# Performance work log

Measured on AMD Instinct MI355X. Metric: run time of the kernel, lower is better.

The kernel has to match this reference:

```python
import jax, jax.numpy as jnp
import numpy as np

L, B, D = 512, 32, 256  # seq_len, batch (hardcoded 32 in source), in_size == hidden_size
H = D


def setup_inputs() -> dict:
    key = jax.random.key(0)
    ks = jax.random.split(key, 9)
    s_in = 1.0 / np.sqrt(D)
    s_h = 1.0 / np.sqrt(H)
    return {
        "v": jax.random.normal(ks[0], (L, B, D), jnp.float32),
        "h0": jax.random.normal(ks[1], (B, H), jnp.float32),       # torch.randn h
        "Vvec": jax.random.normal(ks[2], (B, H), jnp.float32),     # torch.randn V (squeezed [B,H,1])
        "Wp": jax.random.normal(ks[3], (H, D), jnp.float32) * s_in,   # nn.Linear(D,H,bias=False).weight
        "Wp_": jax.random.normal(ks[4], (H, D), jnp.float32) * s_in,
        "W_ih": jax.random.normal(ks[5], (3 * H, D), jnp.float32) * s_h,  # GRUCell weight_ih
        "W_hh": jax.random.normal(ks[6], (3 * H, H), jnp.float32) * s_h,
        "b_ih": jax.random.normal(ks[7], (3 * H,), jnp.float32) * s_h,
        "b_hh": jax.random.normal(ks[8], (3 * H,), jnp.float32) * s_h,
    }


def _gru_cell(c, h, W_ih, W_hh, b_ih, b_hh):
    # torch.nn.GRUCell math
    gi = c @ W_ih.T + b_ih   # [B, 3H]
    gh = h @ W_hh.T + b_hh   # [B, 3H]
    i_r, i_z, i_n = jnp.split(gi, 3, axis=1)
    h_r, h_z, h_n = jnp.split(gh, 3, axis=1)
    r = jax.nn.sigmoid(i_r + h_r)
    z = jax.nn.sigmoid(i_z + h_z)
    n = jnp.tanh(i_n + r * h_n)
    return (1.0 - z) * n + z * h


def reference(v, h0, Vvec, Wp, Wp_, W_ih, W_hh, b_ih, b_hh):
    # Hoist the two linear projections out of the scan (they don't depend on h).
    xq = jnp.einsum('lbd,hd->lbh', v, Wp)    # Wp(v[i]) for all i
    xv = jnp.einsum('lbd,hd->lbh', v, Wp_)   # Wp_(v), reused every step

    def step(h, xq_i):
        x = jnp.tanh(xq_i[None, :, :] + xv)          # [L, B, H]
        s = jnp.einsum('lbh,bh->bl', x, Vvec)        # attention scores over L
        a = jax.nn.softmax(s, axis=1)                # [B, L]
        c = jnp.einsum('bl,lbd->bd', a, v)           # context [B, D]
        h_new = _gru_cell(c, h, W_ih, W_hh, b_ih, b_hh)
        return h_new, h_new

    _, hs = jax.lax.scan(step, h0, xq)  # hs: [L, B, H]
    # dropout is identity in eval mode
    return hs
```

## Files before the change

kernel.cpp:

```cpp
#include <hip/hip_runtime.h>
#include <stdint.h>


#define C2    2.8853900817779268f
#define LOG2E 1.4426950408889634f

typedef __fp16 f16x2 __attribute__((ext_vector_type(2)));
typedef __fp16 f16x4_t __attribute__((ext_vector_type(4)));
typedef __fp16 f16x8 __attribute__((ext_vector_type(8)));
typedef float f32x4 __attribute__((ext_vector_type(4)));

static __device__ __forceinline__ float rcp_f(float x)  { return __builtin_amdgcn_rcpf(x); }
static __device__ __forceinline__ float exp2_f(float x) { return __builtin_amdgcn_exp2f(x); }

__global__ __launch_bounds__(256) void gemm_nt(
    const float* __restrict__ A, const float* __restrict__ W,
    const float* __restrict__ bias, float* __restrict__ out,
    int N, int expmode)
{
  __shared__ __align__(16) float As[32][68];
  __shared__ __align__(16) float Ws[32][68];
  const int t = threadIdx.x;
  const int tx = t & 15, ty = t >> 4;
  const int n0 = blockIdx.x * 64, m0 = blockIdx.y * 64;
  float acc[4][4] = {};

  for (int k0 = 0; k0 < 256; k0 += 32) {
#pragma unroll
    for (int s = 0; s < 2; ++s) {
      int f = t + s * 256;
      int row = f >> 3, kq = f & 7;
      float4 a = *(const float4*)&A[(size_t)(m0 + row) * 256 + k0 + kq * 4];
      float4 w = *(const float4*)&W[(size_t)(n0 + row) * 256 + k0 + kq * 4];
      As[kq * 4 + 0][row] = a.x; As[kq * 4 + 1][row] = a.y;
      As[kq * 4 + 2][row] = a.z; As[kq * 4 + 3][row] = a.w;
      Ws[kq * 4 + 0][row] = w.x; Ws[kq * 4 + 1][row] = w.y;
      Ws[kq * 4 + 2][row] = w.z; Ws[kq * 4 + 3][row] = w.w;
    }
    __syncthreads();
#pragma unroll
    for (int kk = 0; kk < 32; ++kk) {
      float4 a4 = *(const float4*)&As[kk][ty * 4];
      float4 b4 = *(const float4*)&Ws[kk][tx * 4];
      float av[4] = {a4.x, a4.y, a4.z, a4.w};
      float bv[4] = {b4.x, b4.y, b4.z, b4.w};
#pragma unroll
      for (int r = 0; r < 4; ++r)
#pragma unroll
        for (int c = 0; c < 4; ++c)
          acc[r][c] = fmaf(av[r], bv[c], acc[r][c]);
    }
    __syncthreads();
  }

#pragma unroll
  for (int r = 0; r < 4; ++r) {
    float4 o;
    if (expmode) {
      o.x = exp2_f(C2 * acc[r][0]); o.y = exp2_f(C2 * acc[r][1]);
      o.z = exp2_f(C2 * acc[r][2]); o.w = exp2_f(C2 * acc[r][3]);
    } else {
      float4 bb = *(const float4*)&bias[n0 + tx * 4];
      o.x = acc[r][0] + bb.x; o.y = acc[r][1] + bb.y;
      o.z = acc[r][2] + bb.z; o.w = acc[r][3] + bb.w;
    }
    *(float4*)&out[(size_t)(m0 + ty * 4 + r) * N + n0 + tx * 4] = o;
  }
}

__global__ __launch_bounds__(256) void gemm_gi(
    const float* __restrict__ A, const float* __restrict__ W,
    const float* __restrict__ bih, const float* __restrict__ bhh,
    __fp16* __restrict__ G)
{
  __shared__ __align__(16) float As[32][68];
  __shared__ __align__(16) float Ws[32][68];
  const int t = threadIdx.x;
  const int tx = t & 15, ty = t >> 4;
  const int n0 = blockIdx.x * 64, m0 = blockIdx.y * 64;
  float acc[4][4] = {};

  for (int k0 = 0; k0 < 256; k0 += 32) {
#pragma unroll
    for (int s = 0; s < 2; ++s) {
      int f = t + s * 256;
      int row = f >> 3, kq = f & 7;
      float4 a = *(const float4*)&A[(size_t)(m0 + row) * 256 + k0 + kq * 4];
      float4 w = *(const float4*)&W[(size_t)(n0 + row) * 256 + k0 + kq * 4];
      As[kq * 4 + 0][row] = a.x; As[kq * 4 + 1][row] = a.y;
      As[kq * 4 + 2][row] = a.z; As[kq * 4 + 3][row] = a.w;
      Ws[kq * 4 + 0][row] = w.x; Ws[kq * 4 + 1][row] = w.y;
      Ws[kq * 4 + 2][row] = w.z; Ws[kq * 4 + 3][row] = w.w;
    }
    __syncthreads();
#pragma unroll
    for (int kk = 0; kk < 32; ++kk) {
      float4 a4 = *(const float4*)&As[kk][ty * 4];
      float4 b4 = *(const float4*)&Ws[kk][tx * 4];
      float av[4] = {a4.x, a4.y, a4.z, a4.w};
      float bv[4] = {b4.x, b4.y, b4.z, b4.w};
#pragma unroll
      for (int r = 0; r < 4; ++r)
#pragma unroll
        for (int c = 0; c < 4; ++c)
          acc[r][c] = fmaf(av[r], bv[c], acc[r][c]);
    }
    __syncthreads();
  }

  float bias[4];
#pragma unroll
  for (int c = 0; c < 4; ++c) {
    int n = n0 + tx * 4 + c;
    bias[c] = bih[n] + (n < 512 ? bhh[n] : 0.f);
  }
#pragma unroll
  for (int r = 0; r < 4; ++r) {
    int m = m0 + ty * 4 + r;
    f16x4_t o;
#pragma unroll
    for (int c = 0; c < 4; ++c) o[c] = (__fp16)(acc[r][c] + bias[c]);
    *(f16x4_t*)&G[(size_t)m * 768 + n0 + tx * 4] = o;
  }
}

__global__ __launch_bounds__(256) void score_k(
    const float* __restrict__ Eq, const float* __restrict__ Ev,
    const float* __restrict__ Vvec, float* __restrict__ S)
{
  __shared__ __align__(16) float Eqs[64][68];
  __shared__ __align__(16) float Evs[32][68];
  __shared__ __align__(16) float Vs[256];
  const int t = threadIdx.x;
  const int tx = t & 15, ty = t >> 4;
  const int l0 = blockIdx.x * 32;
  const int i0 = blockIdx.y * 64;
  const int b  = blockIdx.z;

  Vs[t] = -2.0f * Vvec[b * 256 + t];
  float acc[4][2] = {};

  for (int st = 0; st < 4; ++st) {
    const int h0 = st * 64;
#pragma unroll
    for (int s = 0; s < 4; ++s) {
      int f = t + s * 256;
      int row = f >> 4, cq = f & 15;
      *(float4*)&Eqs[row][cq * 4] =
          *(const float4*)&Eq[((size_t)(i0 + row) * 32 + b) * 256 + h0 + cq * 4];
    }
#pragma unroll
    for (int s = 0; s < 2; ++s) {
      int f = t + s * 256;
      int row = f >> 4, cq = f & 15;
      *(float4*)&Evs[row][cq * 4] =
          *(const float4*)&Ev[((size_t)(l0 + row) * 32 + b) * 256 + h0 + cq * 4];
    }
    __syncthreads();
#pragma unroll 4
    for (int k4 = 0; k4 < 16; ++k4) {
      float4 vh = *(const float4*)&Vs[h0 + k4 * 4];
      float4 e0 = *(const float4*)&Evs[tx][k4 * 4];
      float4 e1 = *(const float4*)&Evs[tx + 16][k4 * 4];
#pragma unroll
      for (int r = 0; r < 4; ++r) {
        float4 eq = *(const float4*)&Eqs[ty * 4 + r][k4 * 4];
        acc[r][0] += vh.x * rcp_f(fmaf(eq.x, e0.x, 1.0f));
        acc[r][0] += vh.y * rcp_f(fmaf(eq.y, e0.y, 1.0f));
        acc[r][0] += vh.z * rcp_f(fmaf(eq.z, e0.z, 1.0f));
        acc[r][0] += vh.w * rcp_f(fmaf(eq.w, e0.w, 1.0f));
        acc[r][1] += vh.x * rcp_f(fmaf(eq.x, e1.x, 1.0f));
        acc[r][1] += vh.y * rcp_f(fmaf(eq.y, e1.y, 1.0f));
        acc[r][1] += vh.z * rcp_f(fmaf(eq.z, e1.z, 1.0f));
        acc[r][1] += vh.w * rcp_f(fmaf(eq.w, e1.w, 1.0f));
      }
    }
    __syncthreads();
  }

#pragma unroll
  for (int r = 0; r < 4; ++r) {
    float* ps = &S[((size_t)b * 512 + i0 + ty * 4 + r) * 512 + l0];
    ps[tx]      = acc[r][0];
    ps[tx + 16] = acc[r][1];
  }
}

__global__ __launch_bounds__(64) void softmax_k(float* __restrict__ S)
{
  const int t = threadIdx.x;
  float* row = &S[(size_t)blockIdx.x * 512];
  float x[8];
  float m = -1e30f;
#pragma unroll
  for (int u = 0; u < 8; ++u) { x[u] = row[t + u * 64]; m = fmaxf(m, x[u]); }
#pragma unroll
  for (int o = 32; o; o >>= 1) m = fmaxf(m, __shfl_xor(m, o, 64));
  float sum = 0.f;
#pragma unroll
  for (int u = 0; u < 8; ++u) { x[u] = exp2_f(LOG2E * (x[u] - m)); sum += x[u]; }
#pragma unroll
  for (int o = 32; o; o >>= 1) sum += __shfl_xor(sum, o, 64);
  float inv = rcp_f(sum);
#pragma unroll
  for (int u = 0; u < 8; ++u) row[t + u * 64] = x[u] * inv;
}

__global__ __launch_bounds__(256) void ctx_k(
    const float* __restrict__ Aw, const float* __restrict__ v,
    float* __restrict__ C)
{
  __shared__ __align__(16) float As[32][68];
  __shared__ __align__(16) float Vs[32][68];
  const int t = threadIdx.x, tx = t & 15, ty = t >> 4;
  const int d0 = blockIdx.x * 64, i0 = blockIdx.y * 64, b = blockIdx.z;
  float acc[4][4] = {};

  for (int l0 = 0; l0 < 512; l0 += 32) {
#pragma unroll
    for (int s = 0; s < 2; ++s) {
      int f = t + s * 256;
      int row = f >> 3, lq = f & 7;
      float4 a = *(const float4*)&Aw[((size_t)b * 512 + i0 + row) * 512 + l0 + lq * 4];
      As[lq * 4 + 0][row] = a.x; As[lq * 4 + 1][row] = a.y;
      As[lq * 4 + 2][row] = a.z; As[lq * 4 + 3][row] = a.w;
    }
#pragma unroll
    for (int s = 0; s < 2; ++s) {
      int f = t + s * 256;
      int row = f >> 4, dq = f & 15;
      *(float4*)&Vs[row][dq * 4] =
          *(const float4*)&v[((size_t)(l0 + row) * 32 + b) * 256 + d0 + dq * 4];
    }
    __syncthreads();
#pragma unroll
    for (int kk = 0; kk < 32; ++kk) {
      float4 a4 = *(const float4*)&As[kk][ty * 4];
      float4 b4 = *(const float4*)&Vs[kk][tx * 4];
      float av[4] = {a4.x, a4.y, a4.z, a4.w};
      float bv[4] = {b4.x, b4.y, b4.z, b4.w};
#pragma unroll
      for (int r = 0; r < 4; ++r)
#pragma unroll
        for (int c = 0; c < 4; ++c)
          acc[r][c] = fmaf(av[r], bv[c], acc[r][c]);
    }
    __syncthreads();
  }

#pragma unroll
  for (int r = 0; r < 4; ++r) {
    float4 o = {acc[r][0], acc[r][1], acc[r][2], acc[r][3]};
    *(float4*)&C[((size_t)(i0 + ty * 4 + r) * 32 + b) * 256 + d0 + tx * 4] = o;
  }
}

__global__ __launch_bounds__(512, 1) void gru_k(
    const __fp16* __restrict__ Gi2, const float* __restrict__ Whh,
    const float* __restrict__ bhh, const float* __restrict__ h0,
    float* __restrict__ out)
{
  __shared__ __align__(16) __fp16 hA[2][256];
  const int t = threadIdx.x, wave = t >> 6, lane = t & 63;
  const int quad = lane >> 4, col = lane & 15;
  const int b = blockIdx.x;
  const int jw = wave * 32;

  f16x8 Bf[2][3][8];
#pragma unroll
  for (int p = 0; p < 2; ++p)
#pragma unroll
    for (int g = 0; g < 3; ++g) {
      const float* wrow = &Whh[(size_t)(g * 256 + jw + p * 16 + col) * 256];
#pragma unroll
      for (int kk = 0; kk < 8; ++kk) {
        const float4* wp = (const float4*)&wrow[kk * 32 + quad * 8];
        float4 w0 = wp[0], w1 = wp[1];
        f16x8 f;
        f[0] = (__fp16)w0.x; f[1] = (__fp16)w0.y;
        f[2] = (__fp16)w0.z; f[3] = (__fp16)w0.w;
        f[4] = (__fp16)w1.x; f[5] = (__fp16)w1.y;
        f[6] = (__fp16)w1.z; f[7] = (__fp16)w1.w;
        Bf[p][g][kk] = f;
      }
    }

  float hold[2];
  float bn[2];
#pragma unroll
  for (int p = 0; p < 2; ++p) {
    int j = jw + p * 16 + col;
    bn[p] = bhh[512 + j];
    float h = h0[(size_t)b * 256 + j];
    hold[p] = h;
    if (quad == 0) hA[0][j] = (__fp16)h;
  }
  __syncthreads();

  __fp16 gcur[2][3];
#pragma unroll
  for (int p = 0; p < 2; ++p)
#pragma unroll
    for (int g = 0; g < 3; ++g)
      gcur[p][g] = Gi2[(size_t)b * 768 + g * 256 + jw + p * 16 + col];

  for (int i = 0; i < 512; ++i) {
    __fp16 gnext[2][3];
    {
      int ip = (i + 1 < 512) ? (i + 1) : 511;
#pragma unroll
      for (int p = 0; p < 2; ++p)
#pragma unroll
        for (int g = 0; g < 3; ++g)
          gnext[p][g] =
              Gi2[(size_t)(ip * 32 + b) * 768 + g * 256 + jw + p * 16 + col];
    }

    f32x4 acc[2][3];
#pragma unroll
    for (int p = 0; p < 2; ++p)
#pragma unroll
      for (int g = 0; g < 3; ++g)
        acc[p][g] = (f32x4){0.f, 0.f, 0.f, 0.f};

    const __fp16* hbuf = hA[i & 1];
#pragma unroll
    for (int kk = 0; kk < 8; ++kk) {
      f16x8 a = *(const f16x8*)&hbuf[kk * 32 + quad * 8];
#pragma unroll
      for (int p = 0; p < 2; ++p)
#pragma unroll
        for (int g = 0; g < 3; ++g)
          acc[p][g] = __builtin_amdgcn_mfma_f32_16x16x32_f16(
              a, Bf[p][g][kk], acc[p][g], 0, 0, 0);
    }

    __fp16* hnext = hA[(i + 1) & 1];
#pragma unroll
    for (int p = 0; p < 2; ++p) {
      int j = jw + p * 16 + col;
      float rr = rcp_f(1.f + exp2_f(-LOG2E * ((float)gcur[p][0] + acc[p][0][0])));
      float zz = rcp_f(1.f + exp2_f(-LOG2E * ((float)gcur[p][1] + acc[p][1][0])));
      float na = fmaf(rr, acc[p][2][0] + bn[p], (float)gcur[p][2]);
      float nn = fmaf(-2.f, rcp_f(1.f + exp2_f(C2 * na)), 1.f);
      float h = fmaf(zz, hold[p] - nn, nn);
      hold[p] = h;
      if (quad == 0) {
        out[((size_t)i * 32 + b) * 256 + j] = h;
        hnext[j] = (__fp16)h;
      }
    }
#pragma unroll
    for (int p = 0; p < 2; ++p)
#pragma unroll
      for (int g = 0; g < 3; ++g) gcur[p][g] = gnext[p][g];
    __syncthreads();
  }
}

extern "C" void kernel_launch(void* const* d_in, const int* in_sizes, int n_in,
                              void* d_out, int out_size, void* d_ws, size_t ws_size,
                              hipStream_t stream)
{
  const float* v   = (const float*)d_in[0];
  const float* h0  = (const float*)d_in[1];
  const float* Vv  = (const float*)d_in[2];
  const float* Wp  = (const float*)d_in[3];
  const float* Wp_ = (const float*)d_in[4];
  const float* Wih = (const float*)d_in[5];
  const float* Whh = (const float*)d_in[6];
  const float* bih = (const float*)d_in[7];
  const float* bhh = (const float*)d_in[8];
  float* out = (float*)d_out;
  float* ws  = (float*)d_ws;

  float* Eq = ws;
  float* Ev = ws + 4194304;
  float* S  = ws + 8388608;
  float* C  = ws;
  __fp16* Gi2 = (__fp16*)(ws + 4194304);

  gemm_nt<<<dim3(4, 256), 256, 0, stream>>>(v, Wp,  nullptr, Eq, 256, 1);
  gemm_nt<<<dim3(4, 256), 256, 0, stream>>>(v, Wp_, nullptr, Ev, 256, 1);
  score_k<<<dim3(16, 8, 32), 256, 0, stream>>>(Eq, Ev, Vv, S);
  softmax_k<<<16384, 64, 0, stream>>>(S);
  ctx_k<<<dim3(4, 8, 32), 256, 0, stream>>>(S, v, C);
  gemm_gi<<<dim3(12, 256), 256, 0, stream>>>(C, Wih, bih, bhh, Gi2);
  gru_k<<<32, 512, 0, stream>>>(Gi2, Whh, bhh, h0, out);
}
```

Baseline: 1.058 ms.

## Move projection, context and input-gate GEMMs to fp16 MFMA and fuse projections

Replaces the scalar FP32 tiled GEMMs for the two attention projections, the context product and the GRU input gates with fp16 MFMA 16x16x32 kernels. Operands are converted to half precision while staging into shared memory. The two projection GEMMs are fused into one kernel so v is loaded once, and softmax now packs four rows per 256-thread block with float4 loads. The cost is lower operand precision in these GEMMs, plus transposed fp16 shared-memory stores for v in the context kernel.

```diff
diff --git a/kernel.cpp b/kernel.cpp
--- a/kernel.cpp
+++ b/kernel.cpp
@@ -5,123 +5,166 @@
 #define C2    2.8853900817779268f
 #define LOG2E 1.4426950408889634f
 
-typedef __fp16 f16x2 __attribute__((ext_vector_type(2)));
 typedef __fp16 f16x4_t __attribute__((ext_vector_type(4)));
 typedef __fp16 f16x8 __attribute__((ext_vector_type(8)));
 typedef float f32x4 __attribute__((ext_vector_type(4)));
 
 static __device__ __forceinline__ float rcp_f(float x)  { return __builtin_amdgcn_rcpf(x); }
 static __device__ __forceinline__ float exp2_f(float x) { return __builtin_amdgcn_exp2f(x); }
-
-__global__ __launch_bounds__(256) void gemm_nt(
-    const float* __restrict__ A, const float* __restrict__ W,
-    const float* __restrict__ bias, float* __restrict__ out,
-    int N, int expmode)
-{
-  __shared__ __align__(16) float As[32][68];
-  __shared__ __align__(16) float Ws[32][68];
-  const int t = threadIdx.x;
-  const int tx = t & 15, ty = t >> 4;
+static __device__ __forceinline__ f16x8 cvt8(float4 a, float4 b) {
+  f16x8 f;
+  f[0] = (__fp16)a.x; f[1] = (__fp16)a.y; f[2] = (__fp16)a.z; f[3] = (__fp16)a.w;
+  f[4] = (__fp16)b.x; f[5] = (__fp16)b.y; f[6] = (__fp16)b.z; f[7] = (__fp16)b.w;
+  return f;
+}
+
+
+__global__ __launch_bounds__(256) void proj_k(
+    const float* __restrict__ v, const float* __restrict__ Wp,
+    const float* __restrict__ Wp_, float* __restrict__ Eq,
+    float* __restrict__ Ev)
+{
+  __shared__ __align__(16) __fp16 As[64][40];
+  __shared__ __align__(16) __fp16 Wqs[64][40];
+  __shared__ __align__(16) __fp16 Wvs[64][40];
+  const int t = threadIdx.x, wave = t >> 6, lane = t & 63;
+  const int quad = lane >> 4, col = lane & 15;
   const int n0 = blockIdx.x * 64, m0 = blockIdx.y * 64;
-  float acc[4][4] = {};
-
-  for (int k0 = 0; k0 < 256; k0 += 32) {
-#pragma unroll
-    for (int s = 0; s < 2; ++s) {
-      int f = t + s * 256;
-      int row = f >> 3, kq = f & 7;
-      float4 a = *(const float4*)&A[(size_t)(m0 + row) * 256 + k0 + kq * 4];
-      float4 w = *(const float4*)&W[(size_t)(n0 + row) * 256 + k0 + kq * 4];
-      As[kq * 4 + 0][row] = a.x; As[kq * 4 + 1][row] = a.y;
-      As[kq * 4 + 2][row] = a.z; As[kq * 4 + 3][row] = a.w;
-      Ws[kq * 4 + 0][row] = w.x; Ws[kq * 4 + 1][row] = w.y;
-      Ws[kq * 4 + 2][row] = w.z; Ws[kq * 4 + 3][row] = w.w;
-    }
-    __syncthreads();
-#pragma unroll
-    for (int kk = 0; kk < 32; ++kk) {
-      float4 a4 = *(const float4*)&As[kk][ty * 4];
-      float4 b4 = *(const float4*)&Ws[kk][tx * 4];
-      float av[4] = {a4.x, a4.y, a4.z, a4.w};
-      float bv[4] = {b4.x, b4.y, b4.z, b4.w};
-#pragma unroll
-      for (int r = 0; r < 4; ++r)
-#pragma unroll
-        for (int c = 0; c < 4; ++c)
-          acc[r][c] = fmaf(av[r], bv[c], acc[r][c]);
-    }
-    __syncthreads();
-  }
-
-#pragma unroll
-  for (int r = 0; r < 4; ++r) {
-    float4 o;
-    if (expmode) {
-      o.x = exp2_f(C2 * acc[r][0]); o.y = exp2_f(C2 * acc[r][1]);
-      o.z = exp2_f(C2 * acc[r][2]); o.w = exp2_f(C2 * acc[r][3]);
-    } else {
-      float4 bb = *(const float4*)&bias[n0 + tx * 4];
-      o.x = acc[r][0] + bb.x; o.y = acc[r][1] + bb.y;
-      o.z = acc[r][2] + bb.z; o.w = acc[r][3] + bb.w;
-    }
-    *(float4*)&out[(size_t)(m0 + ty * 4 + r) * N + n0 + tx * 4] = o;
-  }
-}
-
-__global__ __launch_bounds__(256) void gemm_gi(
+  const int srow = t >> 2, skq = t & 3;
+
+  f32x4 accq[4], accv[4];
+#pragma unroll
+  for (int nt = 0; nt < 4; ++nt) {
+    accq[nt] = (f32x4){0.f, 0.f, 0.f, 0.f};
+    accv[nt] = (f32x4){0.f, 0.f, 0.f, 0.f};
+  }
+
+  for (int kc = 0; kc < 8; ++kc) {
+    const int k0 = kc * 32;
+    {
+      const float4* ap = (const float4*)&v[(size_t)(m0 + srow) * 256 + k0 + skq * 8];
+      *(f16x8*)&As[srow][skq * 8] = cvt8(ap[0], ap[1]);
+      const float4* qp = (const float4*)&Wp[(size_t)(n0 + srow) * 256 + k0 + skq * 8];
+      *(f16x8*)&Wqs[srow][skq * 8] = cvt8(qp[0], qp[1]);
+      const float4* vp = (const float4*)&Wp_[(size_t)(n0 + srow) * 256 + k0 + skq * 8];
+      *(f16x8*)&Wvs[srow][skq * 8] = cvt8(vp[0], vp[1]);
+    }
+    __syncthreads();
+    f16x8 a = *(const f16x8*)&As[wave * 16 + col][quad * 8];
+#pragma unroll
+    for (int nt = 0; nt < 4; ++nt) {
+      f16x8 bq = *(const f16x8*)&Wqs[nt * 16 + col][quad * 8];
+      f16x8 bv = *(const f16x8*)&Wvs[nt * 16 + col][quad * 8];
+      accq[nt] = __builtin_amdgcn_mfma_f32_16x16x32_f16(a, bq, accq[nt], 0, 0, 0);
+      accv[nt] = __builtin_amdgcn_mfma_f32_16x16x32_f16(a, bv, accv[nt], 0, 0, 0);
+    }
+    __syncthreads();
+  }
+
+#pragma unroll
+  for (int nt = 0; nt < 4; ++nt)
+#pragma unroll
+    for (int r = 0; r < 4; ++r) {
+      size_t m = m0 + wave * 16 + quad * 4 + r;
+      size_t n = n0 + nt * 16 + col;
+      Eq[m * 256 + n] = exp2_f(C2 * accq[nt][r]);
+      Ev[m * 256 + n] = exp2_f(C2 * accv[nt][r]);
+    }
+}
+
+__global__ __launch_bounds__(256) void gi_k(
     const float* __restrict__ A, const float* __restrict__ W,
     const float* __restrict__ bih, const float* __restrict__ bhh,
     __fp16* __restrict__ G)
 {
-  __shared__ __align__(16) float As[32][68];
-  __shared__ __align__(16) float Ws[32][68];
-  const int t = threadIdx.x;
-  const int tx = t & 15, ty = t >> 4;
+  __shared__ __align__(16) __fp16 As[64][40];
+  __shared__ __align__(16) __fp16 Ws[64][40];
+  const int t = threadIdx.x, wave = t >> 6, lane = t & 63;
+  const int quad = lane >> 4, col = lane & 15;
   const int n0 = blockIdx.x * 64, m0 = blockIdx.y * 64;
-  float acc[4][4] = {};
-
-  for (int k0 = 0; k0 < 256; k0 += 32) {
-#pragma unroll
-    for (int s = 0; s < 2; ++s) {
-      int f = t + s * 256;
-      int row = f >> 3, kq = f & 7;
-      float4 a = *(const float4*)&A[(size_t)(m0 + row) * 256 + k0 + kq * 4];
-      float4 w = *(const float4*)&W[(size_t)(n0 + row) * 256 + k0 + kq * 4];
-      As[kq * 4 + 0][row] = a.x; As[kq * 4 + 1][row] = a.y;
-      As[kq * 4 + 2][row] = a.z; As[kq * 4 + 3][row] = a.w;
-      Ws[kq * 4 + 0][row] = w.x; Ws[kq * 4 + 1][row] = w.y;
-      Ws[kq * 4 + 2][row] = w.z; Ws[kq * 4 + 3][row] = w.w;
-    }
-    __syncthreads();
-#pragma unroll
-    for (int kk = 0; kk < 32; ++kk) {
-      float4 a4 = *(const float4*)&As[kk][ty * 4];
-      float4 b4 = *(const float4*)&Ws[kk][tx * 4];
-      float av[4] = {a4.x, a4.y, a4.z, a4.w};
-      float bv[4] = {b4.x, b4.y, b4.z, b4.w};
-#pragma unroll
-      for (int r = 0; r < 4; ++r)
-#pragma unroll
-        for (int c = 0; c < 4; ++c)
-          acc[r][c] = fmaf(av[r], bv[c], acc[r][c]);
-    }
-    __syncthreads();
-  }
-
-  float bias[4];
-#pragma unroll
-  for (int c = 0; c < 4; ++c) {
-    int n = n0 + tx * 4 + c;
-    bias[c] = bih[n] + (n < 512 ? bhh[n] : 0.f);
-  }
-#pragma unroll
-  for (int r = 0; r < 4; ++r) {
-    int m = m0 + ty * 4 + r;
-    f16x4_t o;
-#pragma unroll
-    for (int c = 0; c < 4; ++c) o[c] = (__fp16)(acc[r][c] + bias[c]);
-    *(f16x4_t*)&G[(size_t)m * 768 + n0 + tx * 4] = o;
-  }
+  const int srow = t >> 2, skq = t & 3;
+
+  f32x4 acc[4];
+#pragma unroll
+  for (int nt = 0; nt < 4; ++nt) acc[nt] = (f32x4){0.f, 0.f, 0.f, 0.f};
+
+  for (int kc = 0; kc < 8; ++kc) {
+    const int k0 = kc * 32;
+    {
+      const float4* ap = (const float4*)&A[(size_t)(m0 + srow) * 256 + k0 + skq * 8];
+      *(f16x8*)&As[srow][skq * 8] = cvt8(ap[0], ap[1]);
+      const float4* wp = (const float4*)&W[(size_t)(n0 + srow) * 256 + k0 + skq * 8];
+      *(f16x8*)&Ws[srow][skq * 8] = cvt8(wp[0], wp[1]);
+    }
+    __syncthreads();
+    f16x8 a = *(const f16x8*)&As[wave * 16 + col][quad * 8];
+#pragma unroll
+    for (int nt = 0; nt < 4; ++nt) {
+      f16x8 b = *(const f16x8*)&Ws[nt * 16 + col][quad * 8];
+      acc[nt] = __builtin_amdgcn_mfma_f32_16x16x32_f16(a, b, acc[nt], 0, 0, 0);
+    }
+    __syncthreads();
+  }
+
+#pragma unroll
+  for (int nt = 0; nt < 4; ++nt) {
+    int n = n0 + nt * 16 + col;
+    float bias = bih[n] + (n < 512 ? bhh[n] : 0.f);
+#pragma unroll
+    for (int r = 0; r < 4; ++r) {
+      size_t m = m0 + wave * 16 + quad * 4 + r;
+      G[m * 768 + n] = (__fp16)(acc[nt][r] + bias);
+    }
+  }
+}
+
+__global__ __launch_bounds__(256) void ctxm_k(
+    const float* __restrict__ Aw, const float* __restrict__ v,
+    float* __restrict__ C)
+{
+  __shared__ __align__(16) __fp16 As[64][40];
+  __shared__ __align__(16) __fp16 Vs[64][40];
+  const int t = threadIdx.x, wave = t >> 6, lane = t & 63;
+  const int quad = lane >> 4, col = lane & 15;
+  const int d0 = blockIdx.x * 64, i0 = blockIdx.y * 64, b = blockIdx.z;
+  const int srow = t >> 2, skq = t & 3;
+  const int vl = t >> 3, vdq = t & 7;
+
+  f32x4 acc[4];
+#pragma unroll
+  for (int nt = 0; nt < 4; ++nt) acc[nt] = (f32x4){0.f, 0.f, 0.f, 0.f};
+
+  for (int kc = 0; kc < 16; ++kc) {
+    const int l0 = kc * 32;
+    {
+      const float4* ap =
+          (const float4*)&Aw[((size_t)b * 512 + i0 + srow) * 512 + l0 + skq * 8];
+      *(f16x8*)&As[srow][skq * 8] = cvt8(ap[0], ap[1]);
+      const float4* vp =
+          (const float4*)&v[((size_t)(l0 + vl) * 32 + b) * 256 + d0 + vdq * 8];
+      float4 v0 = vp[0], v1 = vp[1];
+      float vv[8] = {v0.x, v0.y, v0.z, v0.w, v1.x, v1.y, v1.z, v1.w};
+#pragma unroll
+      for (int e = 0; e < 8; ++e) Vs[vdq * 8 + e][vl] = (__fp16)vv[e];
+    }
+    __syncthreads();
+    f16x8 a = *(const f16x8*)&As[wave * 16 + col][quad * 8];
+#pragma unroll
+    for (int nt = 0; nt < 4; ++nt) {
+      f16x8 bb = *(const f16x8*)&Vs[nt * 16 + col][quad * 8];
+      acc[nt] = __builtin_amdgcn_mfma_f32_16x16x32_f16(a, bb, acc[nt], 0, 0, 0);
+    }
+    __syncthreads();
+  }
+
+#pragma unroll
+  for (int nt = 0; nt < 4; ++nt)
+#pragma unroll
+    for (int r = 0; r < 4; ++r) {
+      size_t i = i0 + wave * 16 + quad * 4 + r;
+      size_t d = d0 + nt * 16 + col;
+      C[(i * 32 + b) * 256 + d] = acc[nt][r];
+    }
 }
 
 __global__ __launch_bounds__(256) void score_k(
@@ -186,73 +229,28 @@
   }
 }
 
-__global__ __launch_bounds__(64) void softmax_k(float* __restrict__ S)
-{
-  const int t = threadIdx.x;
-  float* row = &S[(size_t)blockIdx.x * 512];
-  float x[8];
-  float m = -1e30f;
-#pragma unroll
-  for (int u = 0; u < 8; ++u) { x[u] = row[t + u * 64]; m = fmaxf(m, x[u]); }
+__global__ __launch_bounds__(256) void softmax_k(float* __restrict__ S)
+{
+  const int wave = threadIdx.x >> 6, lane = threadIdx.x & 63;
+  float* row = &S[((size_t)blockIdx.x * 4 + wave) * 512];
+  float4 x0 = *(float4*)&row[lane * 4];
+  float4 x1 = *(float4*)&row[256 + lane * 4];
+  float m = fmaxf(fmaxf(fmaxf(x0.x, x0.y), fmaxf(x0.z, x0.w)),
+                  fmaxf(fmaxf(x1.x, x1.y), fmaxf(x1.z, x1.w)));
 #pragma unroll
   for (int o = 32; o; o >>= 1) m = fmaxf(m, __shfl_xor(m, o, 64));
-  float sum = 0.f;
-#pragma unroll
-  for (int u = 0; u < 8; ++u) { x[u] = exp2_f(LOG2E * (x[u] - m)); sum += x[u]; }
+  x0.x = exp2_f(LOG2E * (x0.x - m)); x0.y = exp2_f(LOG2E * (x0.y - m));
+  x0.z = exp2_f(LOG2E * (x0.z - m)); x0.w = exp2_f(LOG2E * (x0.w - m));
+  x1.x = exp2_f(LOG2E * (x1.x - m)); x1.y = exp2_f(LOG2E * (x1.y - m));
+  x1.z = exp2_f(LOG2E * (x1.z - m)); x1.w = exp2_f(LOG2E * (x1.w - m));
+  float sum = x0.x + x0.y + x0.z + x0.w + x1.x + x1.y + x1.z + x1.w;
 #pragma unroll
   for (int o = 32; o; o >>= 1) sum += __shfl_xor(sum, o, 64);
   float inv = rcp_f(sum);
-#pragma unroll
-  for (int u = 0; u < 8; ++u) row[t + u * 64] = x[u] * inv;
-}
-
-__global__ __launch_bounds__(256) void ctx_k(
-    const float* __restrict__ Aw, const float* __restrict__ v,
-    float* __restrict__ C)
-{
-  __shared__ __align__(16) float As[32][68];
-  __shared__ __align__(16) float Vs[32][68];
-  const int t = threadIdx.x, tx = t & 15, ty = t >> 4;
-  const int d0 = blockIdx.x * 64, i0 = blockIdx.y * 64, b = blockIdx.z;
-  float acc[4][4] = {};
-
-  for (int l0 = 0; l0 < 512; l0 += 32) {
-#pragma unroll
-    for (int s = 0; s < 2; ++s) {
-      int f = t + s * 256;
-      int row = f >> 3, lq = f & 7;
-      float4 a = *(const float4*)&Aw[((size_t)b * 512 + i0 + row) * 512 + l0 + lq * 4];
-      As[lq * 4 + 0][row] = a.x; As[lq * 4 + 1][row] = a.y;
-      As[lq * 4 + 2][row] = a.z; As[lq * 4 + 3][row] = a.w;
-    }
-#pragma unroll
-    for (int s = 0; s < 2; ++s) {
-      int f = t + s * 256;
-      int row = f >> 4, dq = f & 15;
-      *(float4*)&Vs[row][dq * 4] =
-          *(const float4*)&v[((size_t)(l0 + row) * 32 + b) * 256 + d0 + dq * 4];
-    }
-    __syncthreads();
-#pragma unroll
-    for (int kk = 0; kk < 32; ++kk) {
-      float4 a4 = *(const float4*)&As[kk][ty * 4];
-      float4 b4 = *(const float4*)&Vs[kk][tx * 4];
-      float av[4] = {a4.x, a4.y, a4.z, a4.w};
-      float bv[4] = {b4.x, b4.y, b4.z, b4.w};
-#pragma unroll
-      for (int r = 0; r < 4; ++r)
-#pragma unroll
-        for (int c = 0; c < 4; ++c)
-          acc[r][c] = fmaf(av[r], bv[c], acc[r][c]);
-    }
-    __syncthreads();
-  }
-
-#pragma unroll
-  for (int r = 0; r < 4; ++r) {
-    float4 o = {acc[r][0], acc[r][1], acc[r][2], acc[r][3]};
-    *(float4*)&C[((size_t)(i0 + ty * 4 + r) * 32 + b) * 256 + d0 + tx * 4] = o;
-  }
+  x0.x *= inv; x0.y *= inv; x0.z *= inv; x0.w *= inv;
+  x1.x *= inv; x1.y *= inv; x1.z *= inv; x1.w *= inv;
+  *(float4*)&row[lane * 4] = x0;
+  *(float4*)&row[256 + lane * 4] = x1;
 }
 
 __global__ __launch_bounds__(512, 1) void gru_k(
@@ -275,13 +273,7 @@
 #pragma unroll
       for (int kk = 0; kk < 8; ++kk) {
         const float4* wp = (const float4*)&wrow[kk * 32 + quad * 8];
-        float4 w0 = wp[0], w1 = wp[1];
-        f16x8 f;
-        f[0] = (__fp16)w0.x; f[1] = (__fp16)w0.y;
-        f[2] = (__fp16)w0.z; f[3] = (__fp16)w0.w;
-        f[4] = (__fp16)w1.x; f[5] = (__fp16)w1.y;
-        f[6] = (__fp16)w1.z; f[7] = (__fp16)w1.w;
-        Bf[p][g][kk] = f;
+        Bf[p][g][kk] = cvt8(wp[0], wp[1]);
       }
     }
 
@@ -380,11 +372,10 @@
   float* C  = ws;
   __fp16* Gi2 = (__fp16*)(ws + 4194304);
 
-  gemm_nt<<<dim3(4, 256), 256, 0, stream>>>(v, Wp,  nullptr, Eq, 256, 1);
-  gemm_nt<<<dim3(4, 256), 256, 0, stream>>>(v, Wp_, nullptr, Ev, 256, 1);
+  proj_k<<<dim3(4, 256), 256, 0, stream>>>(v, Wp, Wp_, Eq, Ev);
   score_k<<<dim3(16, 8, 32), 256, 0, stream>>>(Eq, Ev, Vv, S);
-  softmax_k<<<16384, 64, 0, stream>>>(S);
-  ctx_k<<<dim3(4, 8, 32), 256, 0, stream>>>(S, v, C);
-  gemm_gi<<<dim3(12, 256), 256, 0, stream>>>(C, Wih, bih, bhh, Gi2);
+  softmax_k<<<4096, 256, 0, stream>>>(S);
+  ctxm_k<<<dim3(4, 8, 32), 256, 0, stream>>>(S, v, C);
+  gi_k<<<dim3(12, 256), 256, 0, stream>>>(C, Wih, bih, bhh, Gi2);
   gru_k<<<32, 512, 0, stream>>>(Gi2, Whh, bhh, h0, out);
 }
```

Measured after the change: 940.3 us. -11.1%, faster.
